# Performance work log

Hardware: AMD Instinct MI355X
Metric: run time of the kernel (lower is better)

Reference implementation:

```python
import jax, jax.numpy as jnp
import numpy as np

B, N, D, H = 256, 1000, 128, 8
DH = D // H
TANH_CLIP = 10.0
NEG = -1e9  # finite stand-in for -inf mask fill (keeps grads clean)


def setup_inputs() -> dict:
    key = jax.random.key(0)
    ks = jax.random.split(key, 8)
    s = 1.0 / np.sqrt(D)
    return {
        "node_embeddings": jax.random.normal(ks[0], (B, N, D), jnp.float32),
        "W_node": jax.random.normal(ks[1], (D, 3 * D), jnp.float32) * s,   # project_node_embeddings
        "W_fixed": jax.random.normal(ks[2], (D, D), jnp.float32) * s,      # project_fixed_context
        "W_step": jax.random.normal(ks[3], (2 * D, D), jnp.float32) * s,   # project_step_context
        "W_out": jax.random.normal(ks[4], (D, D), jnp.float32) * s,        # project_out
        "prev_idx": jax.random.randint(ks[5], (B,), 0, N),
        "first_idx": jax.random.randint(ks[6], (B,), 0, N),
        "mask": jax.random.randint(ks[7], (B, N), 0, 2).astype(bool),      # True = masked/visited
    }


def reference(node_embeddings, W_node, W_fixed, W_step, W_out, prev_idx, first_idx, mask):
    b = jnp.arange(B)
    # Precompute fixed: context projection of graph embedding (mean aggregation)
    graph_embed = node_embeddings.mean(axis=1)                    # (B, D)
    fixed_context = graph_embed @ W_fixed                          # (B, D)
    # glimpse key / glimpse val / logit key from node embeddings
    kvl = node_embeddings @ W_node                                 # (B, N, 3D)
    glimpse_K, glimpse_V, logit_K = jnp.split(kvl, 3, axis=-1)
    gK = glimpse_K.reshape(B, N, H, DH)                            # (B, N, H, dh)
    gV = glimpse_V.reshape(B, N, H, DH)
    # Step context: cat(first node embed, last node embed) -> query
    step_ctx = jnp.concatenate(
        [node_embeddings[b, first_idx], node_embeddings[b, prev_idx]], axis=-1)  # (B, 2D)
    query = fixed_context + step_ctx @ W_step                      # (B, D)
    Q = query.reshape(B, H, DH)                                    # (B, H, dh)
    # Glimpse MHA (single query per batch element)
    compat = jnp.einsum("bhd,bnhd->bhn", Q, gK) / np.sqrt(DH)      # (B, H, N)
    compat = jnp.where(mask[:, None, :], NEG, compat)              # mask_inner
    attn = jax.nn.softmax(compat, axis=-1)
    heads = jnp.einsum("bhn,bnhd->bhd", attn, gV)                  # (B, H, dh)
    glimpse = heads.reshape(B, D) @ W_out                          # (B, D)
    # Logits against logit_K, tanh clipping, mask_logits, log-softmax
    logits = jnp.einsum("bd,bnd->bn", glimpse, logit_K) / np.sqrt(D)
    logits = TANH_CLIP * jnp.tanh(logits)
    logits = jnp.where(mask, NEG, logits)
    log_p = jax.nn.log_softmax(logits, axis=-1)                    # (B, N)
    return log_p
```

## Files before the change

kernel.cpp:

```cpp
#include <hip/hip_runtime.h>
#include <math.h>

#define BB 256
#define NN 1000
#define DD 128
#define HH 8
#define NEG -1e9f

__device__ __forceinline__ float bf2f(unsigned int u) {
    return __uint_as_float(u << 16);
}
__device__ __forceinline__ unsigned short f2bf(float f) {
    unsigned int u = __float_as_uint(f);
    u += 0x7FFFu + ((u >> 16) & 1u);
    return (unsigned short)(u >> 16);
}
__device__ __forceinline__ bool get_mask(const void* m, int flag, size_t idx) {
    if (flag == 1) return ((const int*)m)[idx] != 0;
    if (flag == 2) return ((const float*)m)[idx] != 0.0f;
    return ((const unsigned char*)m)[idx] != 0;
}

template<int BF16>
__global__ __launch_bounds__(1024) void k_fused(
        const float* __restrict__ X, const float* __restrict__ Wnode,
        const float* __restrict__ Wfix, const float* __restrict__ Wstep,
        const float* __restrict__ Wout, const int* __restrict__ prev,
        const int* __restrict__ first, const void* __restrict__ mask,
        unsigned short* __restrict__ Xb, float* __restrict__ out) {
    int b = blockIdx.x, tid = threadIdx.x;

    __shared__ __align__(16) float cm[HH * 1024];
    __shared__ __align__(16) float qkl[HH * DD];
    __shared__ __align__(16) float qpart[8 * DD];
    __shared__ float xa[HH * DD];
    __shared__ float ge[DD], q[DD], sc[2 * DD], hd[DD], gl[DD], gqv[DD];
    __shared__ float red[16], invh[8];
    __shared__ int s_flag;

    const size_t xoff = (size_t)b * NN * DD;

    if (tid < 64) {
        const unsigned int* mw = (const unsigned int*)mask;
        unsigned int a0 = mw[tid], a1 = mw[tid + 64], a2 = mw[tid + 128], a3 = mw[tid + 192];
        int ii = (a0 <= 1u) && (a1 <= 1u) && (a2 <= 1u) && (a3 <= 1u);
        int ff = (a0 == 0u || a0 == 0x3F800000u) && (a1 == 0u || a1 == 0x3F800000u) &&
                 (a2 == 0u || a2 == 0x3F800000u) && (a3 == 0u || a3 == 0x3F800000u);
        int ai = __all(ii), af = __all(ff);
        if (tid == 0) s_flag = ai ? 1 : (af ? 2 : 0);
    }
    if (tid >= 256 && tid < 512) {
        int t = tid - 256;
        int src = (t < DD) ? first[b] : prev[b];
        sc[t] = X[xoff + (size_t)src * DD + (t & 127)];
    }

    {
        float4* red4 = (float4*)cm;
        int c = tid & 31, s = tid >> 5;
        const float4* Xr = (const float4*)(X + xoff);
        float4 acc = make_float4(0.f, 0.f, 0.f, 0.f);
        for (int n = s; n < NN; n += 32) {
            float4 v = Xr[n * 32 + c];
            acc.x += v.x; acc.y += v.y; acc.z += v.z; acc.w += v.w;
            if (BF16) {
                uint2 p;
                p.x = (unsigned)f2bf(v.x) | ((unsigned)f2bf(v.y) << 16);
                p.y = (unsigned)f2bf(v.z) | ((unsigned)f2bf(v.w) << 16);
                ((uint2*)Xb)[(size_t)b * NN * 32 + n * 32 + c] = p;
            }
        }
        red4[s * 32 + c] = acc;
        __syncthreads();
        for (int st = 16; st >= 1; st >>= 1) {
            if (s < st) {
                float4 o = red4[(s + st) * 32 + c];
                float4 r = red4[s * 32 + c];
                r.x += o.x; r.y += o.y; r.z += o.z; r.w += o.w;
                red4[s * 32 + c] = r;
            }
            __syncthreads();
        }
        if (s == 0) {
            float4 r = red4[c];
            ge[4 * c]     = r.x * (1.0f / NN);
            ge[4 * c + 1] = r.y * (1.0f / NN);
            ge[4 * c + 2] = r.z * (1.0f / NN);
            ge[4 * c + 3] = r.w * (1.0f / NN);
        }
        __syncthreads();
    }
    const int flag = s_flag;

    {
        int p = tid >> 7, d = tid & 127;
        float a = 0.f;
        #pragma unroll 4
        for (int k = p * 16; k < p * 16 + 16; ++k) a += ge[k] * Wfix[(size_t)k * DD + d];
        #pragma unroll 4
        for (int k = p * 32; k < p * 32 + 32; ++k) a += sc[k] * Wstep[(size_t)k * DD + d];
        qpart[p * DD + d] = a;
        __syncthreads();
        if (tid < DD) {
            float s = 0.f;
            #pragma unroll
            for (int pp = 0; pp < 8; ++pp) s += qpart[pp * DD + tid];
            q[tid] = s;
        }
        __syncthreads();
        int d2 = tid >> 3, h = tid & 7;
        const float4* wr = (const float4*)(Wnode + (size_t)d2 * 384 + h * 16);
        float a2 = 0.f;
        #pragma unroll
        for (int j4 = 0; j4 < 4; ++j4) {
            float4 w = wr[j4];
            a2 += w.x * q[h * 16 + 4 * j4]     + w.y * q[h * 16 + 4 * j4 + 1]
                + w.z * q[h * 16 + 4 * j4 + 2] + w.w * q[h * 16 + 4 * j4 + 3];
        }
        qkl[h * DD + d2] = 0.25f * a2;
        __syncthreads();
    }

    {
        int g = tid & 7;
        for (int it = 0; it < 8; ++it) {
            int n = it * 128 + (tid >> 3);
            if (n < NN) {
                float acc[HH] = {0.f, 0.f, 0.f, 0.f, 0.f, 0.f, 0.f, 0.f};
                if (BF16) {
                    const uint4* xr = (const uint4*)(Xb + xoff + (size_t)n * DD);
                    uint4 c0 = xr[g], c1 = xr[g + 8];
                    unsigned int wsv[8] = {c0.x, c0.y, c0.z, c0.w, c1.x, c1.y, c1.z, c1.w};
                    #pragma unroll
                    for (int i = 0; i < 8; ++i) {
                        int col = (i < 4) ? (8 * g + 2 * i) : (64 + 8 * g + 2 * (i - 4));
                        float lo = bf2f(wsv[i] & 0xffffu), hi = bf2f(wsv[i] >> 16);
                        #pragma unroll
                        for (int h = 0; h < HH; ++h)
                            acc[h] += lo * qkl[h * DD + col] + hi * qkl[h * DD + col + 1];
                    }
                } else {
                    const float4* xr = (const float4*)(X + xoff + (size_t)n * DD);
                    #pragma unroll
                    for (int i = 0; i < 4; ++i) {
                        float4 v = xr[g + 8 * i];
                        int col = 4 * (g + 8 * i);
                        #pragma unroll
                        for (int h = 0; h < HH; ++h)
                            acc[h] += v.x * qkl[h * DD + col]     + v.y * qkl[h * DD + col + 1]
                                    + v.z * qkl[h * DD + col + 2] + v.w * qkl[h * DD + col + 3];
                    }
                }
                #pragma unroll
                for (int h = 0; h < HH; ++h) {
                    acc[h] += __shfl_xor(acc[h], 1, 8);
                    acc[h] += __shfl_xor(acc[h], 2, 8);
                    acc[h] += __shfl_xor(acc[h], 4, 8);
                }
                bool mk = get_mask(mask, flag, (size_t)b * NN + n);
                cm[g * 1024 + n] = mk ? NEG : acc[g];
            }
        }
        __syncthreads();
    }

    {
        int h = tid >> 7, lane = tid & 127;
        float mx = -INFINITY;
        for (int n = lane; n < NN; n += 128) mx = fmaxf(mx, cm[h * 1024 + n]);
        #pragma unroll
        for (int off = 32; off >= 1; off >>= 1) mx = fmaxf(mx, __shfl_xor(mx, off, 64));
        if ((tid & 63) == 0) red[tid >> 6] = mx;
        __syncthreads();
        float m_h = fmaxf(red[2 * h], red[2 * h + 1]);
        float sm = 0.f;
        for (int n = lane; n < NN; n += 128) {
            float p = expf(cm[h * 1024 + n] - m_h);
            cm[h * 1024 + n] = p;
            sm += p;
        }
        #pragma unroll
        for (int off = 32; off >= 1; off >>= 1) sm += __shfl_xor(sm, off, 64);
        __syncthreads();
        if ((tid & 63) == 0) red[tid >> 6] = sm;
        __syncthreads();
        if (tid < HH) invh[tid] = 1.0f / (red[2 * tid] + red[2 * tid + 1]);
        __syncthreads();
    }

    {
        int s = tid >> 7, d = tid & 127;
        float acc[HH] = {0.f, 0.f, 0.f, 0.f, 0.f, 0.f, 0.f, 0.f};
        for (int n = s; n < NN; n += 8) {
            float x = BF16 ? bf2f((unsigned int)Xb[xoff + (size_t)n * DD + d])
                           : X[xoff + (size_t)n * DD + d];
            #pragma unroll
            for (int h = 0; h < HH; ++h) acc[h] += cm[h * 1024 + n] * x;
        }
        __syncthreads();
        float* xp = cm;
        #pragma unroll
        for (int h = 0; h < HH; ++h) xp[(s * HH + h) * DD + d] = acc[h];
        __syncthreads();
        if (s == 0) {
            #pragma unroll
            for (int h = 0; h < HH; ++h) {
                float t = 0.f;
                #pragma unroll
                for (int ss = 0; ss < 8; ++ss) t += xp[(ss * HH + h) * DD + d];
                xa[h * DD + d] = t * invh[h];
            }
        }
        __syncthreads();
    }

    {
        int p = tid >> 7, t = tid & 127;
        int h = t >> 4;
        float a = 0.f;
        #pragma unroll 4
        for (int d = p * 16; d < p * 16 + 16; ++d)
            a += xa[h * DD + d] * Wnode[(size_t)d * 384 + 128 + t];
        qpart[p * DD + t] = a;
        __syncthreads();
        if (tid < DD) {
            float s = 0.f;
            #pragma unroll
            for (int pp = 0; pp < 8; ++pp) s += qpart[pp * DD + tid];
            hd[tid] = s;
        }
        __syncthreads();
        a = 0.f;
        #pragma unroll 4
        for (int k = p * 16; k < p * 16 + 16; ++k) a += hd[k] * Wout[(size_t)k * DD + t];
        qpart[p * DD + t] = a;
        __syncthreads();
        if (tid < DD) {
            float s = 0.f;
            #pragma unroll
            for (int pp = 0; pp < 8; ++pp) s += qpart[pp * DD + tid];
            gl[tid] = s;
        }
        __syncthreads();
        const float4* wr = (const float4*)(Wnode + (size_t)t * 384 + 256 + p * 16);
        a = 0.f;
        #pragma unroll
        for (int j4 = 0; j4 < 4; ++j4) {
            float4 w = wr[j4];
            int k = p * 16 + 4 * j4;
            a += w.x * gl[k] + w.y * gl[k + 1] + w.z * gl[k + 2] + w.w * gl[k + 3];
        }
        qpart[p * DD + t] = a;
        __syncthreads();
        if (tid < DD) {
            float s = 0.f;
            #pragma unroll
            for (int pp = 0; pp < 8; ++pp) s += qpart[pp * DD + tid];
            gqv[tid] = s * 0.08838834764831845f;
        }
        __syncthreads();
    }

    {
        float* lg = qkl;
        int g = tid & 7;
        for (int it = 0; it < 8; ++it) {
            int n = it * 128 + (tid >> 3);
            if (n < NN) {
                float a = 0.f;
                if (BF16) {
                    const uint4* xr = (const uint4*)(Xb + xoff + (size_t)n * DD);
                    uint4 c0 = xr[g], c1 = xr[g + 8];
                    unsigned int wsv[8] = {c0.x, c0.y, c0.z, c0.w, c1.x, c1.y, c1.z, c1.w};
                    #pragma unroll
                    for (int i = 0; i < 8; ++i) {
                        int col = (i < 4) ? (8 * g + 2 * i) : (64 + 8 * g + 2 * (i - 4));
                        a += bf2f(wsv[i] & 0xffffu) * gqv[col] + bf2f(wsv[i] >> 16) * gqv[col + 1];
                    }
                } else {
                    const float4* xr = (const float4*)(X + xoff + (size_t)n * DD);
                    #pragma unroll
                    for (int i = 0; i < 4; ++i) {
                        float4 v = xr[g + 8 * i];
                        int col = 4 * (g + 8 * i);
                        a += v.x * gqv[col] + v.y * gqv[col + 1] + v.z * gqv[col + 2] + v.w * gqv[col + 3];
                    }
                }
                a += __shfl_xor(a, 1, 8);
                a += __shfl_xor(a, 2, 8);
                a += __shfl_xor(a, 4, 8);
                if (g == 0) {
                    float lgt = 10.0f * tanhf(a);
                    lg[n] = get_mask(mask, flag, (size_t)b * NN + n) ? NEG : lgt;
                }
            }
        }
        __syncthreads();
        float v = (tid < NN) ? lg[tid] : -INFINITY;
        float mx = v;
        #pragma unroll
        for (int off = 32; off >= 1; off >>= 1) mx = fmaxf(mx, __shfl_xor(mx, off, 64));
        if ((tid & 63) == 0) red[tid >> 6] = mx;
        __syncthreads();
        float m = red[0];
        #pragma unroll
        for (int w = 1; w < 16; ++w) m = fmaxf(m, red[w]);
        float e = (tid < NN) ? expf(v - m) : 0.f;
        float sm = e;
        #pragma unroll
        for (int off = 32; off >= 1; off >>= 1) sm += __shfl_xor(sm, off, 64);
        __syncthreads();
        if ((tid & 63) == 0) red[tid >> 6] = sm;
        __syncthreads();
        float s2 = 0.f;
        #pragma unroll
        for (int w = 0; w < 16; ++w) s2 += red[w];
        float lse = m + logf(s2);
        if (tid < NN) out[(size_t)b * NN + tid] = v - lse;
    }
}

extern "C" void kernel_launch(void* const* d_in, const int* in_sizes, int n_in,
                              void* d_out, int out_size, void* d_ws, size_t ws_size,
                              hipStream_t stream) {
    const float* X     = (const float*)d_in[0];
    const float* Wnode = (const float*)d_in[1];
    const float* Wfix  = (const float*)d_in[2];
    const float* Wstep = (const float*)d_in[3];
    const float* Wout  = (const float*)d_in[4];
    const int*   prev  = (const int*)d_in[5];
    const int*   first = (const int*)d_in[6];
    const void*  mask  = d_in[7];
    float* out = (float*)d_out;

    const size_t need = 256 + (size_t)2 * BB * NN * DD;
    if (ws_size >= need) {
        unsigned short* Xb = (unsigned short*)((char*)d_ws + 256);
        k_fused<1><<<BB, 1024, 0, stream>>>(X, Wnode, Wfix, Wstep, Wout,
                                            prev, first, mask, Xb, out);
    } else {
        k_fused<0><<<BB, 1024, 0, stream>>>(X, Wnode, Wfix, Wstep, Wout,
                                            prev, first, mask, nullptr, out);
    }
}
```

Before: 109.4 us.

## Split fused kernel into multi-kernel flash-style pipeline over node chunks

Replaces the single 1024-thread block per batch with four kernels: a chunked mean reduction, a per-quarter attention kernel that saves partial max/sum/PV values, an output kernel that merges the partials and computes logits per quarter, and a final normalisation kernel. The bf16 copy of X is dropped, so every pass reads fp32 X directly. The goal is to spread each batch across more, smaller blocks (1024 instead of 256) and fill the GPU better. In exchange there are extra launches and workspace round trips, X is re-read several times in fp32, the query projection is recomputed in every quarter block, and log-softmax uses a fixed max of 10.

```diff
diff --git a/kernel.cpp b/kernel.cpp
--- a/kernel.cpp
+++ b/kernel.cpp
@@ -5,151 +5,134 @@
 #define NN 1000
 #define DD 128
 #define HH 8
+#define QQ 4
+#define RQ 250
 #define NEG -1e9f
 
-__device__ __forceinline__ float bf2f(unsigned int u) {
-    return __uint_as_float(u << 16);
-}
-__device__ __forceinline__ unsigned short f2bf(float f) {
-    unsigned int u = __float_as_uint(f);
-    u += 0x7FFFu + ((u >> 16) & 1u);
-    return (unsigned short)(u >> 16);
-}
 __device__ __forceinline__ bool get_mask(const void* m, int flag, size_t idx) {
     if (flag == 1) return ((const int*)m)[idx] != 0;
     if (flag == 2) return ((const float*)m)[idx] != 0.0f;
     return ((const unsigned char*)m)[idx] != 0;
 }
 
-template<int BF16>
-__global__ __launch_bounds__(1024) void k_fused(
-        const float* __restrict__ X, const float* __restrict__ Wnode,
-        const float* __restrict__ Wfix, const float* __restrict__ Wstep,
-        const float* __restrict__ Wout, const int* __restrict__ prev,
-        const int* __restrict__ first, const void* __restrict__ mask,
-        unsigned short* __restrict__ Xb, float* __restrict__ out) {
-    int b = blockIdx.x, tid = threadIdx.x;
-
-    __shared__ __align__(16) float cm[HH * 1024];
-    __shared__ __align__(16) float qkl[HH * DD];
-    __shared__ __align__(16) float qpart[8 * DD];
-    __shared__ float xa[HH * DD];
-    __shared__ float ge[DD], q[DD], sc[2 * DD], hd[DD], gl[DD], gqv[DD];
-    __shared__ float red[16], invh[8];
-    __shared__ int s_flag;
-
-    const size_t xoff = (size_t)b * NN * DD;
-
-    if (tid < 64) {
-        const unsigned int* mw = (const unsigned int*)mask;
-        unsigned int a0 = mw[tid], a1 = mw[tid + 64], a2 = mw[tid + 128], a3 = mw[tid + 192];
+__global__ __launch_bounds__(256) void k_mean(
+        const float* __restrict__ X, float* __restrict__ partial,
+        const unsigned int* __restrict__ maskw, int* __restrict__ flag) {
+    int bid = blockIdx.x, tid = threadIdx.x;
+    int b = bid >> 3, ch = bid & 7;
+    if (bid == 0 && tid < 64) {
+        unsigned int a0 = maskw[tid], a1 = maskw[tid + 64],
+                     a2 = maskw[tid + 128], a3 = maskw[tid + 192];
         int ii = (a0 <= 1u) && (a1 <= 1u) && (a2 <= 1u) && (a3 <= 1u);
         int ff = (a0 == 0u || a0 == 0x3F800000u) && (a1 == 0u || a1 == 0x3F800000u) &&
                  (a2 == 0u || a2 == 0x3F800000u) && (a3 == 0u || a3 == 0x3F800000u);
         int ai = __all(ii), af = __all(ff);
-        if (tid == 0) s_flag = ai ? 1 : (af ? 2 : 0);
-    }
-    if (tid >= 256 && tid < 512) {
-        int t = tid - 256;
-        int src = (t < DD) ? first[b] : prev[b];
-        sc[t] = X[xoff + (size_t)src * DD + (t & 127)];
-    }
-
-    {
-        float4* red4 = (float4*)cm;
-        int c = tid & 31, s = tid >> 5;
-        const float4* Xr = (const float4*)(X + xoff);
-        float4 acc = make_float4(0.f, 0.f, 0.f, 0.f);
-        for (int n = s; n < NN; n += 32) {
-            float4 v = Xr[n * 32 + c];
-            acc.x += v.x; acc.y += v.y; acc.z += v.z; acc.w += v.w;
-            if (BF16) {
-                uint2 p;
-                p.x = (unsigned)f2bf(v.x) | ((unsigned)f2bf(v.y) << 16);
-                p.y = (unsigned)f2bf(v.z) | ((unsigned)f2bf(v.w) << 16);
-                ((uint2*)Xb)[(size_t)b * NN * 32 + n * 32 + c] = p;
+        if (tid == 0) *flag = ai ? 1 : (af ? 2 : 0);
+    }
+    int c = tid & 31, s = tid >> 5;
+    const float4* Xr = (const float4*)(X + (size_t)b * NN * DD);
+    float4 acc = make_float4(0.f, 0.f, 0.f, 0.f);
+    int n0 = ch * 125, n1 = n0 + 125;
+    for (int n = n0 + s; n < n1; n += 8) {
+        float4 v = Xr[n * 32 + c];
+        acc.x += v.x; acc.y += v.y; acc.z += v.z; acc.w += v.w;
+    }
+    __shared__ float4 red[8][32];
+    red[s][c] = acc;
+    __syncthreads();
+    for (int st = 4; st >= 1; st >>= 1) {
+        if (s < st) {
+            float4 o = red[s + st][c];
+            red[s][c].x += o.x; red[s][c].y += o.y;
+            red[s][c].z += o.z; red[s][c].w += o.w;
+        }
+        __syncthreads();
+    }
+    if (s == 0) {
+        float4 r = red[0][c];
+        float* outp = partial + ((size_t)b * 8 + ch) * DD + 4 * c;
+        outp[0] = r.x; outp[1] = r.y; outp[2] = r.z; outp[3] = r.w;
+    }
+}
+
+__global__ __launch_bounds__(256) void k_flash(
+        const float* __restrict__ X, const float* __restrict__ Wnode,
+        const float* __restrict__ Wfix, const float* __restrict__ Wstep,
+        const int* __restrict__ prev, const int* __restrict__ first,
+        const void* __restrict__ mask, const int* __restrict__ flag,
+        const float* __restrict__ partial, float* __restrict__ mqw,
+        float* __restrict__ sqw, float* __restrict__ pvp) {
+    int bid = blockIdx.x, tid = threadIdx.x;
+    int b = bid >> 2, q = bid & 3;
+    const size_t xoff = (size_t)b * NN * DD;
+    const int f = *flag;
+
+    __shared__ float ge[DD], sc[2 * DD], qv[DD];
+    __shared__ float qpart[2][DD];
+    __shared__ float qk[HH][DD];
+    __shared__ float cm[HH][264];
+    __shared__ float mloc[HH];
+
+    if (tid < DD) {
+        float g = 0.f;
+        #pragma unroll
+        for (int ch = 0; ch < 8; ++ch) g += partial[((size_t)b * 8 + ch) * DD + tid];
+        ge[tid] = g * (1.0f / NN);
+    }
+    {
+        int src = (tid < DD) ? first[b] : prev[b];
+        sc[tid] = X[xoff + (size_t)src * DD + (tid & 127)];
+    }
+    __syncthreads();
+
+    {
+        int p = tid >> 7, d = tid & 127;
+        float a = 0.f;
+        #pragma unroll 4
+        for (int k = p * 64; k < p * 64 + 64; ++k)   a += ge[k] * Wfix[(size_t)k * DD + d];
+        #pragma unroll 4
+        for (int k = p * 128; k < p * 128 + 128; ++k) a += sc[k] * Wstep[(size_t)k * DD + d];
+        qpart[p][d] = a;
+    }
+    __syncthreads();
+    if (tid < DD) qv[tid] = qpart[0][tid] + qpart[1][tid];
+    __syncthreads();
+
+    {
+        int hg = tid >> 7, d = tid & 127;
+        const float* wrow = Wnode + (size_t)d * 384;
+        #pragma unroll
+        for (int h = hg * 4; h < hg * 4 + 4; ++h) {
+            const float4* wr = (const float4*)(wrow + h * 16);
+            float a = 0.f;
+            #pragma unroll
+            for (int j4 = 0; j4 < 4; ++j4) {
+                float4 w = wr[j4];
+                a += w.x * qv[h * 16 + 4 * j4]     + w.y * qv[h * 16 + 4 * j4 + 1]
+                   + w.z * qv[h * 16 + 4 * j4 + 2] + w.w * qv[h * 16 + 4 * j4 + 3];
             }
-        }
-        red4[s * 32 + c] = acc;
-        __syncthreads();
-        for (int st = 16; st >= 1; st >>= 1) {
-            if (s < st) {
-                float4 o = red4[(s + st) * 32 + c];
-                float4 r = red4[s * 32 + c];
-                r.x += o.x; r.y += o.y; r.z += o.z; r.w += o.w;
-                red4[s * 32 + c] = r;
-            }
-            __syncthreads();
-        }
-        if (s == 0) {
-            float4 r = red4[c];
-            ge[4 * c]     = r.x * (1.0f / NN);
-            ge[4 * c + 1] = r.y * (1.0f / NN);
-            ge[4 * c + 2] = r.z * (1.0f / NN);
-            ge[4 * c + 3] = r.w * (1.0f / NN);
-        }
-        __syncthreads();
-    }
-    const int flag = s_flag;
-
-    {
-        int p = tid >> 7, d = tid & 127;
-        float a = 0.f;
-        #pragma unroll 4
-        for (int k = p * 16; k < p * 16 + 16; ++k) a += ge[k] * Wfix[(size_t)k * DD + d];
-        #pragma unroll 4
-        for (int k = p * 32; k < p * 32 + 32; ++k) a += sc[k] * Wstep[(size_t)k * DD + d];
-        qpart[p * DD + d] = a;
-        __syncthreads();
-        if (tid < DD) {
-            float s = 0.f;
-            #pragma unroll
-            for (int pp = 0; pp < 8; ++pp) s += qpart[pp * DD + tid];
-            q[tid] = s;
-        }
-        __syncthreads();
-        int d2 = tid >> 3, h = tid & 7;
-        const float4* wr = (const float4*)(Wnode + (size_t)d2 * 384 + h * 16);
-        float a2 = 0.f;
-        #pragma unroll
-        for (int j4 = 0; j4 < 4; ++j4) {
-            float4 w = wr[j4];
-            a2 += w.x * q[h * 16 + 4 * j4]     + w.y * q[h * 16 + 4 * j4 + 1]
-                + w.z * q[h * 16 + 4 * j4 + 2] + w.w * q[h * 16 + 4 * j4 + 3];
-        }
-        qkl[h * DD + d2] = 0.25f * a2;
-        __syncthreads();
-    }
-
-    {
-        int g = tid & 7;
+            qk[h][d] = 0.25f * a;
+        }
+    }
+    __syncthreads();
+
+    const int n0 = q * RQ;
+    {
+        int g = tid & 7, r = tid >> 3;
         for (int it = 0; it < 8; ++it) {
-            int n = it * 128 + (tid >> 3);
-            if (n < NN) {
+            int nl = it * 32 + r;
+            if (nl < RQ) {
+                int n = n0 + nl;
+                const float4* xr = (const float4*)(X + xoff + (size_t)n * DD);
                 float acc[HH] = {0.f, 0.f, 0.f, 0.f, 0.f, 0.f, 0.f, 0.f};
-                if (BF16) {
-                    const uint4* xr = (const uint4*)(Xb + xoff + (size_t)n * DD);
-                    uint4 c0 = xr[g], c1 = xr[g + 8];
-                    unsigned int wsv[8] = {c0.x, c0.y, c0.z, c0.w, c1.x, c1.y, c1.z, c1.w};
+                #pragma unroll
+                for (int i = 0; i < 4; ++i) {
+                    float4 v = xr[g + 8 * i];
+                    int col = 4 * (g + 8 * i);
                     #pragma unroll
-                    for (int i = 0; i < 8; ++i) {
-                        int col = (i < 4) ? (8 * g + 2 * i) : (64 + 8 * g + 2 * (i - 4));
-                        float lo = bf2f(wsv[i] & 0xffffu), hi = bf2f(wsv[i] >> 16);
-                        #pragma unroll
-                        for (int h = 0; h < HH; ++h)
-                            acc[h] += lo * qkl[h * DD + col] + hi * qkl[h * DD + col + 1];
-                    }
-                } else {
-                    const float4* xr = (const float4*)(X + xoff + (size_t)n * DD);
-                    #pragma unroll
-                    for (int i = 0; i < 4; ++i) {
-                        float4 v = xr[g + 8 * i];
-                        int col = 4 * (g + 8 * i);
-                        #pragma unroll
-                        for (int h = 0; h < HH; ++h)
-                            acc[h] += v.x * qkl[h * DD + col]     + v.y * qkl[h * DD + col + 1]
-                                    + v.z * qkl[h * DD + col + 2] + v.w * qkl[h * DD + col + 3];
-                    }
+                    for (int h = 0; h < HH; ++h)
+                        acc[h] += v.x * qk[h][col]     + v.y * qk[h][col + 1]
+                                + v.z * qk[h][col + 2] + v.w * qk[h][col + 3];
                 }
                 #pragma unroll
                 for (int h = 0; h < HH; ++h) {
@@ -157,167 +140,184 @@
                     acc[h] += __shfl_xor(acc[h], 2, 8);
                     acc[h] += __shfl_xor(acc[h], 4, 8);
                 }
-                bool mk = get_mask(mask, flag, (size_t)b * NN + n);
-                cm[g * 1024 + n] = mk ? NEG : acc[g];
+                float val = acc[0];
+                #pragma unroll
+                for (int h = 1; h < HH; ++h) val = (g == h) ? acc[h] : val;
+                bool mk = get_mask(mask, f, (size_t)b * NN + n);
+                cm[g][nl] = mk ? NEG : val;
             }
         }
+    }
+    __syncthreads();
+
+    {
+        int h = tid >> 5, l = tid & 31;
+        float mx = -INFINITY;
+        for (int nl = l; nl < RQ; nl += 32) mx = fmaxf(mx, cm[h][nl]);
+        #pragma unroll
+        for (int off = 16; off >= 1; off >>= 1) mx = fmaxf(mx, __shfl_xor(mx, off, 32));
+        if (l == 0) mloc[h] = mx;
+    }
+    __syncthreads();
+
+    {
+        int h = tid >> 5, l = tid & 31;
+        float m_h = mloc[h];
+        float sm = 0.f;
+        for (int nl = l; nl < RQ; nl += 32) {
+            float p = __expf(cm[h][nl] - m_h);
+            cm[h][nl] = p;
+            sm += p;
+        }
+        #pragma unroll
+        for (int off = 16; off >= 1; off >>= 1) sm += __shfl_xor(sm, off, 32);
+        if (l == 0) {
+            sqw[((size_t)b * QQ + q) * HH + h] = sm;
+            mqw[((size_t)b * QQ + q) * HH + h] = m_h;
+        }
+    }
+    __syncthreads();
+
+    {
+        int s2 = tid >> 7, d = tid & 127;
+        float accp[HH] = {0.f, 0.f, 0.f, 0.f, 0.f, 0.f, 0.f, 0.f};
+        for (int nl = s2; nl < RQ; nl += 2) {
+            float x = X[xoff + (size_t)(n0 + nl) * DD + d];
+            #pragma unroll
+            for (int h = 0; h < HH; ++h) accp[h] += cm[h][nl] * x;
+        }
         __syncthreads();
-    }
-
-    {
-        int h = tid >> 7, lane = tid & 127;
-        float mx = -INFINITY;
-        for (int n = lane; n < NN; n += 128) mx = fmaxf(mx, cm[h * 1024 + n]);
-        #pragma unroll
-        for (int off = 32; off >= 1; off >>= 1) mx = fmaxf(mx, __shfl_xor(mx, off, 64));
-        if ((tid & 63) == 0) red[tid >> 6] = mx;
+        float* cmf = &cm[0][0];
+        #pragma unroll
+        for (int h = 0; h < HH; ++h) cmf[(s2 * HH + h) * DD + d] = accp[h];
         __syncthreads();
-        float m_h = fmaxf(red[2 * h], red[2 * h + 1]);
-        float sm = 0.f;
-        for (int n = lane; n < NN; n += 128) {
-            float p = expf(cm[h * 1024 + n] - m_h);
-            cm[h * 1024 + n] = p;
-            sm += p;
-        }
-        #pragma unroll
-        for (int off = 32; off >= 1; off >>= 1) sm += __shfl_xor(sm, off, 64);
-        __syncthreads();
-        if ((tid & 63) == 0) red[tid >> 6] = sm;
-        __syncthreads();
-        if (tid < HH) invh[tid] = 1.0f / (red[2 * tid] + red[2 * tid + 1]);
-        __syncthreads();
-    }
-
-    {
-        int s = tid >> 7, d = tid & 127;
-        float acc[HH] = {0.f, 0.f, 0.f, 0.f, 0.f, 0.f, 0.f, 0.f};
-        for (int n = s; n < NN; n += 8) {
-            float x = BF16 ? bf2f((unsigned int)Xb[xoff + (size_t)n * DD + d])
-                           : X[xoff + (size_t)n * DD + d];
+        if (s2 == 0) {
             #pragma unroll
-            for (int h = 0; h < HH; ++h) acc[h] += cm[h * 1024 + n] * x;
-        }
-        __syncthreads();
-        float* xp = cm;
-        #pragma unroll
-        for (int h = 0; h < HH; ++h) xp[(s * HH + h) * DD + d] = acc[h];
-        __syncthreads();
-        if (s == 0) {
+            for (int h = 0; h < HH; ++h)
+                pvp[(((size_t)b * QQ + q) * HH + h) * DD + d] =
+                    cmf[h * DD + d] + cmf[(HH + h) * DD + d];
+        }
+    }
+}
+
+__global__ __launch_bounds__(256) void k_out(
+        const float* __restrict__ X, const float* __restrict__ Wnode,
+        const float* __restrict__ Wout, const void* __restrict__ mask,
+        const int* __restrict__ flag, const float* __restrict__ mqw,
+        const float* __restrict__ sqw, const float* __restrict__ pvp,
+        float* __restrict__ lg, float* __restrict__ ssum) {
+    int bid = blockIdx.x, tid = threadIdx.x;
+    int b = bid >> 2, q = bid & 3;
+    const size_t xoff = (size_t)b * NN * DD;
+    const int f = *flag;
+
+    __shared__ float wq[QQ][HH], Sh[HH];
+    __shared__ float xa[HH][DD];
+    __shared__ float qpart[2][DD], hd[DD], gl[DD], gqv[DD];
+    __shared__ float redw[4];
+
+    if (tid < HH) {
+        float m = mqw[((size_t)b * QQ) * HH + tid];
+        #pragma unroll
+        for (int qq = 1; qq < QQ; ++qq)
+            m = fmaxf(m, mqw[((size_t)b * QQ + qq) * HH + tid]);
+        float S = 0.f;
+        #pragma unroll
+        for (int qq = 0; qq < QQ; ++qq) {
+            float wgt = __expf(mqw[((size_t)b * QQ + qq) * HH + tid] - m);
+            wq[qq][tid] = wgt;
+            S += sqw[((size_t)b * QQ + qq) * HH + tid] * wgt;
+        }
+        Sh[tid] = 1.0f / S;
+    }
+    __syncthreads();
+    for (int idx = tid; idx < HH * DD; idx += 256) {
+        int h = idx >> 7, d = idx & 127;
+        float a = 0.f;
+        #pragma unroll
+        for (int qq = 0; qq < QQ; ++qq)
+            a += pvp[(((size_t)b * QQ + qq) * HH + h) * DD + d] * wq[qq][h];
+        xa[h][d] = a * Sh[h];
+    }
+    __syncthreads();
+
+    int p = tid >> 7, t = tid & 127;
+    {
+        int h = t >> 4;
+        float a = 0.f;
+        #pragma unroll 4
+        for (int d = p * 64; d < p * 64 + 64; ++d)
+            a += xa[h][d] * Wnode[(size_t)d * 384 + 128 + t];
+        qpart[p][t] = a;
+    }
+    __syncthreads();
+    if (tid < DD) hd[tid] = qpart[0][tid] + qpart[1][tid];
+    __syncthreads();
+    {
+        float a = 0.f;
+        #pragma unroll 4
+        for (int k = p * 64; k < p * 64 + 64; ++k) a += hd[k] * Wout[(size_t)k * DD + t];
+        qpart[p][t] = a;
+    }
+    __syncthreads();
+    if (tid < DD) gl[tid] = qpart[0][tid] + qpart[1][tid];
+    __syncthreads();
+    {
+        const float4* wr = (const float4*)(Wnode + (size_t)t * 384 + 256 + p * 64);
+        float a = 0.f;
+        #pragma unroll
+        for (int j4 = 0; j4 < 16; ++j4) {
+            float4 w = wr[j4];
+            int k = p * 64 + 4 * j4;
+            a += w.x * gl[k] + w.y * gl[k + 1] + w.z * gl[k + 2] + w.w * gl[k + 3];
+        }
+        qpart[p][t] = a;
+    }
+    __syncthreads();
+    if (tid < DD) gqv[tid] = (qpart[0][tid] + qpart[1][tid]) * 0.08838834764831845f;
+    __syncthreads();
+
+    int g = tid & 7, r = tid >> 3;
+    float esum = 0.f;
+    for (int it = 0; it < 8; ++it) {
+        int nl = it * 32 + r;
+        if (nl < RQ) {
+            int n = q * RQ + nl;
+            const float4* xr = (const float4*)(X + xoff + (size_t)n * DD);
+            float a = 0.f;
             #pragma unroll
-            for (int h = 0; h < HH; ++h) {
-                float t = 0.f;
-                #pragma unroll
-                for (int ss = 0; ss < 8; ++ss) t += xp[(ss * HH + h) * DD + d];
-                xa[h * DD + d] = t * invh[h];
+            for (int i = 0; i < 4; ++i) {
+                float4 v = xr[g + 8 * i];
+                int col = 4 * (g + 8 * i);
+                a += v.x * gqv[col] + v.y * gqv[col + 1] + v.z * gqv[col + 2] + v.w * gqv[col + 3];
             }
-        }
-        __syncthreads();
-    }
-
-    {
-        int p = tid >> 7, t = tid & 127;
-        int h = t >> 4;
-        float a = 0.f;
-        #pragma unroll 4
-        for (int d = p * 16; d < p * 16 + 16; ++d)
-            a += xa[h * DD + d] * Wnode[(size_t)d * 384 + 128 + t];
-        qpart[p * DD + t] = a;
-        __syncthreads();
-        if (tid < DD) {
-            float s = 0.f;
-            #pragma unroll
-            for (int pp = 0; pp < 8; ++pp) s += qpart[pp * DD + tid];
-            hd[tid] = s;
-        }
-        __syncthreads();
-        a = 0.f;
-        #pragma unroll 4
-        for (int k = p * 16; k < p * 16 + 16; ++k) a += hd[k] * Wout[(size_t)k * DD + t];
-        qpart[p * DD + t] = a;
-        __syncthreads();
-        if (tid < DD) {
-            float s = 0.f;
-            #pragma unroll
-            for (int pp = 0; pp < 8; ++pp) s += qpart[pp * DD + tid];
-            gl[tid] = s;
-        }
-        __syncthreads();
-        const float4* wr = (const float4*)(Wnode + (size_t)t * 384 + 256 + p * 16);
-        a = 0.f;
-        #pragma unroll
-        for (int j4 = 0; j4 < 4; ++j4) {
-            float4 w = wr[j4];
-            int k = p * 16 + 4 * j4;
-            a += w.x * gl[k] + w.y * gl[k + 1] + w.z * gl[k + 2] + w.w * gl[k + 3];
-        }
-        qpart[p * DD + t] = a;
-        __syncthreads();
-        if (tid < DD) {
-            float s = 0.f;
-            #pragma unroll
-            for (int pp = 0; pp < 8; ++pp) s += qpart[pp * DD + tid];
-            gqv[tid] = s * 0.08838834764831845f;
-        }
-        __syncthreads();
-    }
-
-    {
-        float* lg = qkl;
-        int g = tid & 7;
-        for (int it = 0; it < 8; ++it) {
-            int n = it * 128 + (tid >> 3);
-            if (n < NN) {
-                float a = 0.f;
-                if (BF16) {
-                    const uint4* xr = (const uint4*)(Xb + xoff + (size_t)n * DD);
-                    uint4 c0 = xr[g], c1 = xr[g + 8];
-                    unsigned int wsv[8] = {c0.x, c0.y, c0.z, c0.w, c1.x, c1.y, c1.z, c1.w};
-                    #pragma unroll
-                    for (int i = 0; i < 8; ++i) {
-                        int col = (i < 4) ? (8 * g + 2 * i) : (64 + 8 * g + 2 * (i - 4));
-                        a += bf2f(wsv[i] & 0xffffu) * gqv[col] + bf2f(wsv[i] >> 16) * gqv[col + 1];
-                    }
-                } else {
-                    const float4* xr = (const float4*)(X + xoff + (size_t)n * DD);
-                    #pragma unroll
-                    for (int i = 0; i < 4; ++i) {
-                        float4 v = xr[g + 8 * i];
-                        int col = 4 * (g + 8 * i);
-                        a += v.x * gqv[col] + v.y * gqv[col + 1] + v.z * gqv[col + 2] + v.w * gqv[col + 3];
-                    }
-                }
-                a += __shfl_xor(a, 1, 8);
-                a += __shfl_xor(a, 2, 8);
-                a += __shfl_xor(a, 4, 8);
-                if (g == 0) {
-                    float lgt = 10.0f * tanhf(a);
-                    lg[n] = get_mask(mask, flag, (size_t)b * NN + n) ? NEG : lgt;
-                }
+            a += __shfl_xor(a, 1, 8);
+            a += __shfl_xor(a, 2, 8);
+            a += __shfl_xor(a, 4, 8);
+            if (g == 0) {
+                float l = 10.0f * tanhf(a);
+                if (get_mask(mask, f, (size_t)b * NN + n)) l = NEG;
+                lg[(size_t)b * NN + n] = l;
+                esum += __expf(l - 10.0f);
             }
         }
-        __syncthreads();
-        float v = (tid < NN) ? lg[tid] : -INFINITY;
-        float mx = v;
-        #pragma unroll
-        for (int off = 32; off >= 1; off >>= 1) mx = fmaxf(mx, __shfl_xor(mx, off, 64));
-        if ((tid & 63) == 0) red[tid >> 6] = mx;
-        __syncthreads();
-        float m = red[0];
-        #pragma unroll
-        for (int w = 1; w < 16; ++w) m = fmaxf(m, red[w]);
-        float e = (tid < NN) ? expf(v - m) : 0.f;
-        float sm = e;
-        #pragma unroll
-        for (int off = 32; off >= 1; off >>= 1) sm += __shfl_xor(sm, off, 64);
-        __syncthreads();
-        if ((tid & 63) == 0) red[tid >> 6] = sm;
-        __syncthreads();
-        float s2 = 0.f;
-        #pragma unroll
-        for (int w = 0; w < 16; ++w) s2 += red[w];
-        float lse = m + logf(s2);
-        if (tid < NN) out[(size_t)b * NN + tid] = v - lse;
-    }
+    }
+    #pragma unroll
+    for (int off = 32; off >= 1; off >>= 1) esum += __shfl_xor(esum, off, 64);
+    if ((tid & 63) == 0) redw[tid >> 6] = esum;
+    __syncthreads();
+    if (tid == 0) ssum[(size_t)b * QQ + q] = redw[0] + redw[1] + redw[2] + redw[3];
+}
+
+__global__ __launch_bounds__(256) void k_final(
+        const float* __restrict__ lg, const float* __restrict__ ssum,
+        float* __restrict__ out) {
+    int b = blockIdx.x, tid = threadIdx.x;
+    float s = ssum[(size_t)b * QQ] + ssum[(size_t)b * QQ + 1]
+            + ssum[(size_t)b * QQ + 2] + ssum[(size_t)b * QQ + 3];
+    float lse = 10.0f + logf(s);
+    for (int n = tid; n < NN; n += 256)
+        out[(size_t)b * NN + n] = lg[(size_t)b * NN + n] - lse;
 }
 
 extern "C" void kernel_launch(void* const* d_in, const int* in_sizes, int n_in,
@@ -333,13 +333,19 @@
     const void*  mask  = d_in[7];
     float* out = (float*)d_out;
 
-    const size_t need = 256 + (size_t)2 * BB * NN * DD;
-    if (ws_size >= need) {
-        unsigned short* Xb = (unsigned short*)((char*)d_ws + 256);
-        k_fused<1><<<BB, 1024, 0, stream>>>(X, Wnode, Wfix, Wstep, Wout,
-                                            prev, first, mask, Xb, out);
-    } else {
-        k_fused<0><<<BB, 1024, 0, stream>>>(X, Wnode, Wfix, Wstep, Wout,
-                                            prev, first, mask, nullptr, out);
-    }
-}
+    int*   flag    = (int*)d_ws;
+    float* w       = (float*)d_ws;
+    float* ssum    = w + 16;
+    float* partial = ssum + BB * QQ;
+    float* mqw     = partial + (size_t)BB * 8 * DD;
+    float* sqw     = mqw + (size_t)BB * QQ * HH;
+    float* pvp     = sqw + (size_t)BB * QQ * HH;
+    float* lg      = pvp + (size_t)BB * QQ * HH * DD;
+
+    k_mean <<<BB * 8, 256, 0, stream>>>(X, partial, (const unsigned int*)mask, flag);
+    k_flash<<<BB * QQ, 256, 0, stream>>>(X, Wnode, Wfix, Wstep, prev, first, mask,
+                                         flag, partial, mqw, sqw, pvp);
+    k_out  <<<BB * QQ, 256, 0, stream>>>(X, Wnode, Wout, mask, flag, mqw, sqw, pvp,
+                                         lg, ssum);
+    k_final<<<BB, 256, 0, stream>>>(lg, ssum, out);
+}
```

Result: slower. 149.6 us (+36.8%).

## Split each batch row across four cooperative blocks with grid-wide syncs

Applied to the files above, without the earlier changes.

Adds a cooperative kernel that splits each batch element's 1000 nodes over four 256-thread blocks, giving 1024 blocks instead of 256. Partial sums for the mean, the per-head softmax max and sum, the weighted value sums and the logit exp-sums go to workspace and are merged after grid.sync barriers. It also uses a fixed shift of 10 (the tanh clip bound) for the final log-softmax so no global max pass is needed, and switches expf to __expf. The goal is better CU occupancy and parallelism, at the cost of three grid barriers, extra global traffic for the partials, and a fallback path if the cooperative launch fails.

```diff
diff --git a/kernel.cpp b/kernel.cpp
--- a/kernel.cpp
+++ b/kernel.cpp
@@ -1,10 +1,15 @@
 #include <hip/hip_runtime.h>
+#include <hip/hip_cooperative_groups.h>
 #include <math.h>
+
+namespace cg = cooperative_groups;
 
 #define BB 256
 #define NN 1000
 #define DD 128
 #define HH 8
+#define QQ 4
+#define RQ 250
 #define NEG -1e9f
 
 __device__ __forceinline__ float bf2f(unsigned int u) {
@@ -22,6 +27,355 @@
 }
 
 template<int BF16>
+__global__ __launch_bounds__(256, 4) void k_coop(
+        const float* __restrict__ X, const float* __restrict__ Wnode,
+        const float* __restrict__ Wfix, const float* __restrict__ Wstep,
+        const float* __restrict__ Wout, const int* __restrict__ prev,
+        const int* __restrict__ first, const void* __restrict__ mask,
+        int* __restrict__ flag, float* __restrict__ partial,
+        float* __restrict__ mqw, float* __restrict__ sqw,
+        float* __restrict__ pvp, float* __restrict__ ssum,
+        unsigned short* __restrict__ Xb, float* __restrict__ out) {
+    cg::grid_group grid = cg::this_grid();
+    const int bid = blockIdx.x, tid = threadIdx.x;
+    const int b = bid >> 2, q = bid & 3;
+    const int n0 = q * RQ;
+    const size_t xoff = (size_t)b * NN * DD;
+
+    __shared__ __align__(16) unsigned char pool[16384];
+    __shared__ float cm[HH][264];
+    float4* red4 = (float4*)pool;
+    float*  ge   = (float*)(pool + 4096);
+    float*  sc   = (float*)(pool + 4608);
+    float*  qv   = (float*)(pool + 5632);
+    float*  qpart= (float*)(pool + 6144);
+    float*  qk   = (float*)(pool + 7168);
+    float*  mloc = (float*)(pool + 11264);
+    float*  xp   = (float*)pool;
+    float*  wq   = (float*)pool;
+    float*  Sh   = (float*)(pool + 128);
+    float*  xa   = (float*)(pool + 512);
+    float*  hd   = (float*)(pool + 4608);
+    float*  gl   = (float*)(pool + 5120);
+    float*  gqv  = (float*)(pool + 5632);
+    float*  lgl  = (float*)(pool + 6144);
+    float*  redw = (float*)(pool + 7200);
+
+    if (bid == 0 && tid < 64) {
+        const unsigned int* mw = (const unsigned int*)mask;
+        unsigned int a0 = mw[tid], a1 = mw[tid + 64], a2 = mw[tid + 128], a3 = mw[tid + 192];
+        int ii = (a0 <= 1u) && (a1 <= 1u) && (a2 <= 1u) && (a3 <= 1u);
+        int ff = (a0 == 0u || a0 == 0x3F800000u) && (a1 == 0u || a1 == 0x3F800000u) &&
+                 (a2 == 0u || a2 == 0x3F800000u) && (a3 == 0u || a3 == 0x3F800000u);
+        int ai = __all(ii), af = __all(ff);
+        if (tid == 0) *flag = ai ? 1 : (af ? 2 : 0);
+    }
+    {
+        int c = tid & 31, s = tid >> 5;
+        const float4* Xr = (const float4*)(X + xoff);
+        float4 acc = make_float4(0.f, 0.f, 0.f, 0.f);
+        for (int nl = s; nl < RQ; nl += 8) {
+            int n = n0 + nl;
+            float4 v = Xr[n * 32 + c];
+            acc.x += v.x; acc.y += v.y; acc.z += v.z; acc.w += v.w;
+            if (BF16) {
+                uint2 p;
+                p.x = (unsigned)f2bf(v.x) | ((unsigned)f2bf(v.y) << 16);
+                p.y = (unsigned)f2bf(v.z) | ((unsigned)f2bf(v.w) << 16);
+                ((uint2*)Xb)[((size_t)b * NN + n) * 32 + c] = p;
+            }
+        }
+        red4[s * 32 + c] = acc;
+        __syncthreads();
+        for (int st = 4; st >= 1; st >>= 1) {
+            if (s < st) {
+                float4 o = red4[(s + st) * 32 + c];
+                float4 r = red4[s * 32 + c];
+                r.x += o.x; r.y += o.y; r.z += o.z; r.w += o.w;
+                red4[s * 32 + c] = r;
+            }
+            __syncthreads();
+        }
+        if (s == 0) {
+            float4 r = red4[c];
+            float* outp = partial + ((size_t)b * QQ + q) * DD + 4 * c;
+            outp[0] = r.x; outp[1] = r.y; outp[2] = r.z; outp[3] = r.w;
+        }
+    }
+    grid.sync();
+
+    const int f = *flag;
+    if (tid < DD) {
+        float g = 0.f;
+        #pragma unroll
+        for (int qq = 0; qq < QQ; ++qq) g += partial[((size_t)b * QQ + qq) * DD + tid];
+        ge[tid] = g * (1.0f / NN);
+    }
+    {
+        int src = (tid < DD) ? first[b] : prev[b];
+        sc[tid] = X[xoff + (size_t)src * DD + (tid & 127)];
+    }
+    __syncthreads();
+    {
+        int p = tid >> 7, d = tid & 127;
+        float a = 0.f;
+        #pragma unroll 4
+        for (int k = p * 64; k < p * 64 + 64; ++k)     a += ge[k] * Wfix[(size_t)k * DD + d];
+        #pragma unroll 4
+        for (int k = p * 128; k < p * 128 + 128; ++k)  a += sc[k] * Wstep[(size_t)k * DD + d];
+        qpart[p * DD + d] = a;
+    }
+    __syncthreads();
+    if (tid < DD) qv[tid] = qpart[tid] + qpart[DD + tid];
+    __syncthreads();
+    {
+        int hg = tid >> 7, d = tid & 127;
+        const float* wrow = Wnode + (size_t)d * 384;
+        #pragma unroll
+        for (int h = hg * 4; h < hg * 4 + 4; ++h) {
+            const float4* wr = (const float4*)(wrow + h * 16);
+            float a = 0.f;
+            #pragma unroll
+            for (int j4 = 0; j4 < 4; ++j4) {
+                float4 w = wr[j4];
+                a += w.x * qv[h * 16 + 4 * j4]     + w.y * qv[h * 16 + 4 * j4 + 1]
+                   + w.z * qv[h * 16 + 4 * j4 + 2] + w.w * qv[h * 16 + 4 * j4 + 3];
+            }
+            qk[h * DD + d] = 0.25f * a;
+        }
+    }
+    __syncthreads();
+    {
+        int g = tid & 7, r = tid >> 3;
+        for (int it = 0; it < 8; ++it) {
+            int nl = it * 32 + r;
+            if (nl < RQ) {
+                int n = n0 + nl;
+                float acc[HH] = {0.f, 0.f, 0.f, 0.f, 0.f, 0.f, 0.f, 0.f};
+                if (BF16) {
+                    const uint4* xr = (const uint4*)(Xb + ((size_t)b * NN + n) * DD);
+                    uint4 c0 = xr[g], c1 = xr[g + 8];
+                    unsigned int wsv[8] = {c0.x, c0.y, c0.z, c0.w, c1.x, c1.y, c1.z, c1.w};
+                    #pragma unroll
+                    for (int i = 0; i < 8; ++i) {
+                        int col = (i < 4) ? (8 * g + 2 * i) : (64 + 8 * g + 2 * (i - 4));
+                        float lo = bf2f(wsv[i] & 0xffffu), hi = bf2f(wsv[i] >> 16);
+                        #pragma unroll
+                        for (int h = 0; h < HH; ++h)
+                            acc[h] += lo * qk[h * DD + col] + hi * qk[h * DD + col + 1];
+                    }
+                } else {
+                    const float4* xr = (const float4*)(X + xoff + (size_t)n * DD);
+                    #pragma unroll
+                    for (int i = 0; i < 4; ++i) {
+                        float4 v = xr[g + 8 * i];
+                        int col = 4 * (g + 8 * i);
+                        #pragma unroll
+                        for (int h = 0; h < HH; ++h)
+                            acc[h] += v.x * qk[h * DD + col]     + v.y * qk[h * DD + col + 1]
+                                    + v.z * qk[h * DD + col + 2] + v.w * qk[h * DD + col + 3];
+                    }
+                }
+                #pragma unroll
+                for (int h = 0; h < HH; ++h) {
+                    acc[h] += __shfl_xor(acc[h], 1, 8);
+                    acc[h] += __shfl_xor(acc[h], 2, 8);
+                    acc[h] += __shfl_xor(acc[h], 4, 8);
+                }
+                float val = acc[0];
+                #pragma unroll
+                for (int h = 1; h < HH; ++h) val = (g == h) ? acc[h] : val;
+                bool mk = get_mask(mask, f, (size_t)b * NN + n);
+                cm[g][nl] = mk ? NEG : val;
+            }
+        }
+    }
+    __syncthreads();
+    {
+        int h = tid >> 5, l = tid & 31;
+        float mx = -INFINITY;
+        for (int nl = l; nl < RQ; nl += 32) mx = fmaxf(mx, cm[h][nl]);
+        #pragma unroll
+        for (int off = 16; off >= 1; off >>= 1) mx = fmaxf(mx, __shfl_xor(mx, off, 32));
+        if (l == 0) mloc[h] = mx;
+    }
+    __syncthreads();
+    {
+        int h = tid >> 5, l = tid & 31;
+        float m_h = mloc[h];
+        float sm = 0.f;
+        for (int nl = l; nl < RQ; nl += 32) {
+            float p = __expf(cm[h][nl] - m_h);
+            cm[h][nl] = p;
+            sm += p;
+        }
+        #pragma unroll
+        for (int off = 16; off >= 1; off >>= 1) sm += __shfl_xor(sm, off, 32);
+        if (l == 0) {
+            sqw[((size_t)b * QQ + q) * HH + h] = sm;
+            mqw[((size_t)b * QQ + q) * HH + h] = m_h;
+        }
+    }
+    __syncthreads();
+    {
+        int s4 = tid >> 6, dp = tid & 63;
+        float a0[HH] = {0.f, 0.f, 0.f, 0.f, 0.f, 0.f, 0.f, 0.f};
+        float a1[HH] = {0.f, 0.f, 0.f, 0.f, 0.f, 0.f, 0.f, 0.f};
+        for (int nl = s4; nl < RQ; nl += 4) {
+            float x0, x1;
+            if (BF16) {
+                unsigned int u = *(const unsigned int*)
+                    (Xb + ((size_t)b * NN + n0 + nl) * DD + 2 * dp);
+                x0 = bf2f(u & 0xffffu); x1 = bf2f(u >> 16);
+            } else {
+                float2 v = *(const float2*)(X + xoff + (size_t)(n0 + nl) * DD + 2 * dp);
+                x0 = v.x; x1 = v.y;
+            }
+            #pragma unroll
+            for (int h = 0; h < HH; ++h) {
+                float p = cm[h][nl];
+                a0[h] += p * x0; a1[h] += p * x1;
+            }
+        }
+        #pragma unroll
+        for (int h = 0; h < HH; ++h) {
+            xp[((size_t)s4 * HH + h) * DD + 2 * dp]     = a0[h];
+            xp[((size_t)s4 * HH + h) * DD + 2 * dp + 1] = a1[h];
+        }
+        __syncthreads();
+        if (s4 == 0) {
+            #pragma unroll
+            for (int h = 0; h < HH; ++h) {
+                float t0 = 0.f, t1 = 0.f;
+                #pragma unroll
+                for (int ss = 0; ss < 4; ++ss) {
+                    t0 += xp[((size_t)ss * HH + h) * DD + 2 * dp];
+                    t1 += xp[((size_t)ss * HH + h) * DD + 2 * dp + 1];
+                }
+                pvp[(((size_t)b * QQ + q) * HH + h) * DD + 2 * dp]     = t0;
+                pvp[(((size_t)b * QQ + q) * HH + h) * DD + 2 * dp + 1] = t1;
+            }
+        }
+    }
+    grid.sync();
+
+    if (tid < HH) {
+        float m = mqw[((size_t)b * QQ) * HH + tid];
+        #pragma unroll
+        for (int qq = 1; qq < QQ; ++qq)
+            m = fmaxf(m, mqw[((size_t)b * QQ + qq) * HH + tid]);
+        float S = 0.f;
+        #pragma unroll
+        for (int qq = 0; qq < QQ; ++qq) {
+            float wgt = __expf(mqw[((size_t)b * QQ + qq) * HH + tid] - m);
+            wq[qq * HH + tid] = wgt;
+            S += sqw[((size_t)b * QQ + qq) * HH + tid] * wgt;
+        }
+        Sh[tid] = 1.0f / S;
+    }
+    __syncthreads();
+    for (int idx = tid; idx < HH * DD; idx += 256) {
+        int h = idx >> 7, d = idx & 127;
+        float a = 0.f;
+        #pragma unroll
+        for (int qq = 0; qq < QQ; ++qq)
+            a += pvp[(((size_t)b * QQ + qq) * HH + h) * DD + d] * wq[qq * HH + h];
+        xa[h * DD + d] = a * Sh[h];
+    }
+    __syncthreads();
+    {
+        int p = tid >> 7, t = tid & 127;
+        {
+            int h = t >> 4;
+            float a = 0.f;
+            #pragma unroll 4
+            for (int d = p * 64; d < p * 64 + 64; ++d)
+                a += xa[h * DD + d] * Wnode[(size_t)d * 384 + 128 + t];
+            qpart[p * DD + t] = a;
+        }
+        __syncthreads();
+        if (tid < DD) hd[tid] = qpart[tid] + qpart[DD + tid];
+        __syncthreads();
+        {
+            float a = 0.f;
+            #pragma unroll 4
+            for (int k = p * 64; k < p * 64 + 64; ++k) a += hd[k] * Wout[(size_t)k * DD + t];
+            qpart[p * DD + t] = a;
+        }
+        __syncthreads();
+        if (tid < DD) gl[tid] = qpart[tid] + qpart[DD + tid];
+        __syncthreads();
+        {
+            const float4* wr = (const float4*)(Wnode + (size_t)t * 384 + 256 + p * 64);
+            float a = 0.f;
+            #pragma unroll
+            for (int j4 = 0; j4 < 16; ++j4) {
+                float4 w = wr[j4];
+                int k = p * 64 + 4 * j4;
+                a += w.x * gl[k] + w.y * gl[k + 1] + w.z * gl[k + 2] + w.w * gl[k + 3];
+            }
+            qpart[p * DD + t] = a;
+        }
+        __syncthreads();
+        if (tid < DD) gqv[tid] = (qpart[tid] + qpart[DD + tid]) * 0.08838834764831845f;
+    }
+    __syncthreads();
+    {
+        int g = tid & 7, r = tid >> 3;
+        float esum = 0.f;
+        for (int it = 0; it < 8; ++it) {
+            int nl = it * 32 + r;
+            if (nl < RQ) {
+                int n = n0 + nl;
+                float a = 0.f;
+                if (BF16) {
+                    const uint4* xr = (const uint4*)(Xb + ((size_t)b * NN + n) * DD);
+                    uint4 c0 = xr[g], c1 = xr[g + 8];
+                    unsigned int wsv[8] = {c0.x, c0.y, c0.z, c0.w, c1.x, c1.y, c1.z, c1.w};
+                    #pragma unroll
+                    for (int i = 0; i < 8; ++i) {
+                        int col = (i < 4) ? (8 * g + 2 * i) : (64 + 8 * g + 2 * (i - 4));
+                        a += bf2f(wsv[i] & 0xffffu) * gqv[col] + bf2f(wsv[i] >> 16) * gqv[col + 1];
+                    }
+                } else {
+                    const float4* xr = (const float4*)(X + xoff + (size_t)n * DD);
+                    #pragma unroll
+                    for (int i = 0; i < 4; ++i) {
+                        float4 v = xr[g + 8 * i];
+                        int col = 4 * (g + 8 * i);
+                        a += v.x * gqv[col] + v.y * gqv[col + 1]
+                           + v.z * gqv[col + 2] + v.w * gqv[col + 3];
+                    }
+                }
+                a += __shfl_xor(a, 1, 8);
+                a += __shfl_xor(a, 2, 8);
+                a += __shfl_xor(a, 4, 8);
+                if (g == 0) {
+                    float l = 10.0f * tanhf(a);
+                    if (get_mask(mask, f, (size_t)b * NN + n)) l = NEG;
+                    lgl[nl] = l;
+                    esum += __expf(l - 10.0f);
+                }
+            }
+        }
+        #pragma unroll
+        for (int off = 32; off >= 1; off >>= 1) esum += __shfl_xor(esum, off, 64);
+        if ((tid & 63) == 0) redw[tid >> 6] = esum;
+        __syncthreads();
+        if (tid == 0) ssum[(size_t)b * QQ + q] = redw[0] + redw[1] + redw[2] + redw[3];
+    }
+    grid.sync();
+
+    {
+        float s = ssum[(size_t)b * QQ] + ssum[(size_t)b * QQ + 1]
+                + ssum[(size_t)b * QQ + 2] + ssum[(size_t)b * QQ + 3];
+        float lse = 10.0f + logf(s);
+        for (int nl = tid; nl < RQ; nl += 256)
+            out[(size_t)b * NN + n0 + nl] = lgl[nl] - lse;
+    }
+}
+
+template<int BF16>
 __global__ __launch_bounds__(1024) void k_fused(
         const float* __restrict__ X, const float* __restrict__ Wnode,
         const float* __restrict__ Wfix, const float* __restrict__ Wstep,
@@ -96,9 +450,9 @@
         int p = tid >> 7, d = tid & 127;
         float a = 0.f;
         #pragma unroll 4
-        for (int k = p * 16; k < p * 16 + 16; ++k) a += ge[k] * Wfix[(size_t)k * DD + d];
+        for (int k = p * 16; k < p * 16 + 16; ++k) a += ge[k] * Wfix[k * DD + d];
         #pragma unroll 4
-        for (int k = p * 32; k < p * 32 + 32; ++k) a += sc[k] * Wstep[(size_t)k * DD + d];
+        for (int k = p * 32; k < p * 32 + 32; ++k) a += sc[k] * Wstep[k * DD + d];
         qpart[p * DD + d] = a;
         __syncthreads();
         if (tid < DD) {
@@ -157,8 +511,11 @@
                     acc[h] += __shfl_xor(acc[h], 2, 8);
                     acc[h] += __shfl_xor(acc[h], 4, 8);
                 }
+                float val = acc[0];
+                #pragma unroll
+                for (int h = 1; h < HH; ++h) val = (g == h) ? acc[h] : val;
                 bool mk = get_mask(mask, flag, (size_t)b * NN + n);
-                cm[g * 1024 + n] = mk ? NEG : acc[g];
+                cm[g * 1024 + n] = mk ? NEG : val;
             }
         }
         __syncthreads();
@@ -175,7 +532,7 @@
         float m_h = fmaxf(red[2 * h], red[2 * h + 1]);
         float sm = 0.f;
         for (int n = lane; n < NN; n += 128) {
-            float p = expf(cm[h * 1024 + n] - m_h);
+            float p = __expf(cm[h * 1024 + n] - m_h);
             cm[h * 1024 + n] = p;
             sm += p;
         }
@@ -305,7 +662,7 @@
         float m = red[0];
         #pragma unroll
         for (int w = 1; w < 16; ++w) m = fmaxf(m, red[w]);
-        float e = (tid < NN) ? expf(v - m) : 0.f;
+        float e = (tid < NN) ? __expf(v - m) : 0.f;
         float sm = e;
         #pragma unroll
         for (int off = 32; off >= 1; off >>= 1) sm += __shfl_xor(sm, off, 64);
@@ -333,13 +690,46 @@
     const void*  mask  = d_in[7];
     float* out = (float*)d_out;
 
-    const size_t need = 256 + (size_t)2 * BB * NN * DD;
-    if (ws_size >= need) {
-        unsigned short* Xb = (unsigned short*)((char*)d_ws + 256);
-        k_fused<1><<<BB, 1024, 0, stream>>>(X, Wnode, Wfix, Wstep, Wout,
-                                            prev, first, mask, Xb, out);
-    } else {
-        k_fused<0><<<BB, 1024, 0, stream>>>(X, Wnode, Wfix, Wstep, Wout,
-                                            prev, first, mask, nullptr, out);
+    char* wsb = (char*)d_ws;
+    int*   flag    = (int*)wsb;
+    float* partial = (float*)(wsb + 256);
+    float* mqw     = partial + (size_t)BB * QQ * DD;
+    float* sqw     = mqw + (size_t)BB * QQ * HH;
+    float* pvp     = sqw + (size_t)BB * QQ * HH;
+    float* ssum    = pvp + (size_t)BB * QQ * HH * DD;
+    const size_t scratch_end = 256 + sizeof(float) *
+        ((size_t)BB * QQ * DD + 2 * (size_t)BB * QQ * HH +
+         (size_t)BB * QQ * HH * DD + (size_t)BB * QQ);
+    const size_t xb_off = (scratch_end + 255) & ~(size_t)255;
+    unsigned short* Xb = (unsigned short*)(wsb + xb_off);
+    const size_t coop_need_bf16 = xb_off + (size_t)2 * BB * NN * DD;
+
+    bool launched = false;
+    if (ws_size >= scratch_end) {
+        const int want_bf16 = (ws_size >= coop_need_bf16) ? 1 : 0;
+        const void* kptr = want_bf16 ? (const void*)k_coop<1> : (const void*)k_coop<0>;
+        int maxb = 0;
+        if (hipOccupancyMaxActiveBlocksPerMultiprocessor(&maxb, kptr, 256, 0) == hipSuccess
+            && maxb >= 4) {
+            unsigned short* xbp = want_bf16 ? Xb : nullptr;
+            void* args[] = {(void*)&X, (void*)&Wnode, (void*)&Wfix, (void*)&Wstep,
+                            (void*)&Wout, (void*)&prev, (void*)&first, (void*)&mask,
+                            (void*)&flag, (void*)&partial, (void*)&mqw, (void*)&sqw,
+                            (void*)&pvp, (void*)&ssum, (void*)&xbp, (void*)&out};
+            dim3 g(BB * QQ), blk(256);
+            launched = (hipLaunchCooperativeKernel(kptr, g, blk, args, 0, stream)
+                        == hipSuccess);
+        }
+    }
+    if (!launched) {
+        const size_t mega_need = 256 + (size_t)2 * BB * NN * DD;
+        if (ws_size >= mega_need) {
+            unsigned short* Xm = (unsigned short*)(wsb + 256);
+            k_fused<1><<<BB, 1024, 0, stream>>>(X, Wnode, Wfix, Wstep, Wout,
+                                                prev, first, mask, Xm, out);
+        } else {
+            k_fused<0><<<BB, 1024, 0, stream>>>(X, Wnode, Wfix, Wstep, Wout,
+                                                prev, first, mask, nullptr, out);
+        }
     }
 }
```

After: 108.2 us (median of 5 runs). No clear change (-1.1%).
